# Kernel optimization log

Hardware: AMD Instinct MI355X
Metric: run time of the kernel (lower is better)

## Reference

```python
import jax, jax.numpy as jnp
import numpy as np

BAND_WIDTH = 0.5
EPS = 1e-5
NORM_EPS = 1e-12  # F.normalize eps


def setup_inputs() -> dict:
    key = jax.random.key(0)
    k1, k2 = jax.random.split(key)
    shape = (8, 512, 48, 48)  # N, C, H, W  (VGG conv4_4 features of a 384x384 image)
    return {
        "pred": jax.random.normal(k1, shape, dtype=jnp.float32),
        "target": jax.random.normal(k2, shape, dtype=jnp.float32),
    }


def reference(pred, target):
    N, C, H, W = pred.shape
    # center both by target channel-mean over (N, H, W)
    y_mu = jnp.mean(target, axis=(0, 2, 3), keepdims=True)
    x_c = pred - y_mu
    y_c = target - y_mu
    # L2-normalize along channel dim (F.normalize: divide by max(norm, eps))
    x_n = x_c / jnp.maximum(jnp.linalg.norm(x_c, axis=1, keepdims=True), NORM_EPS)
    y_n = y_c / jnp.maximum(jnp.linalg.norm(y_c, axis=1, keepdims=True), NORM_EPS)
    x_v = x_n.reshape(N, C, H * W)
    y_v = y_n.reshape(N, C, H * W)
    # pairwise cosine distance: [N, HW, HW]
    cosine_sim = jnp.einsum('ncp,ncq->npq', x_v, y_v)
    dist_raw = 1.0 - cosine_sim
    # relative distance: divide each row by its min over keys (dim=2)
    dist_min = jnp.min(dist_raw, axis=2, keepdims=True)
    dist_tilde = dist_raw / (dist_min + EPS)
    # similarity + row-normalize (softmax-like over dim=2)
    w = jnp.exp((1.0 - dist_tilde) / BAND_WIDTH)
    cx = w / jnp.sum(w, axis=2, keepdims=True)
    # max over query dim (dim=1), mean over key dim -> [N]
    cx = jnp.mean(jnp.max(cx, axis=1), axis=1)
    cx_loss = -jnp.log(cx + EPS)
    # reduction='mean', loss_weight=1.0
    return jnp.mean(cx_loss)
```

## Files before the change

### kernel.cpp

```cpp
#include <hip/hip_runtime.h>
#include <stdint.h>

#define NB 8
#define CC 512
#define PP 2304
#define EPSF 1e-5f

typedef short bf16x8 __attribute__((ext_vector_type(8)));
typedef float f32x4 __attribute__((ext_vector_type(4)));

__device__ __forceinline__ float bf2f(uint32_t b16) {
  return __uint_as_float(b16 << 16);
}
__device__ __forceinline__ uint32_t f2bf(float f) {
  uint32_t u = __float_as_uint(f);
  return (u + 0x7fffu + ((u >> 16) & 1u)) >> 16;
}

__global__ __launch_bounds__(256) void k_chan_mean(const float* __restrict__ tgt,
                                                   float* __restrict__ mu) {
  const int c = blockIdx.x, t = threadIdx.x;
  float s = 0.f;
  for (int n = 0; n < NB; ++n) {
    const float* b = tgt + ((size_t)n * CC + c) * PP;
    for (int p = t; p < PP; p += 256) s += b[p];
  }
  for (int off = 32; off; off >>= 1) s += __shfl_down(s, off);
  __shared__ float red[4];
  if ((t & 63) == 0) red[t >> 6] = s;
  __syncthreads();
  if (t == 0) mu[c] = (red[0] + red[1] + red[2] + red[3]) * (1.0f / (NB * PP));
}

__global__ __launch_bounds__(256) void k_center_cast(
    const float* __restrict__ pred, const float* __restrict__ tgt,
    const float* __restrict__ mu,
    uint16_t* __restrict__ xt, uint16_t* __restrict__ yt,
    float* __restrict__ ssx, float* __restrict__ ssy) {
  __shared__ uint32_t lt[64][33];
  __shared__ float red[4][64];
  const int p0 = blockIdx.x * 64, c0 = blockIdx.y * 64, n = blockIdx.z;
  const int t = threadIdx.x, lp = t & 63, cb = t >> 6;
  for (int which = 0; which < 2; ++which) {
    const float* in = which ? tgt : pred;
    uint16_t* out = which ? yt : xt;
    float* ss = which ? ssy : ssx;
    float sq = 0.f;
    uint32_t packs[8];
#pragma unroll
    for (int i = 0; i < 16; ++i) {
      const int c = c0 + cb * 16 + i;
      float v = in[((size_t)n * CC + c) * PP + p0 + lp] - mu[c];
      sq += v * v;
      uint32_t b = f2bf(v);
      if (i & 1) packs[i >> 1] |= b << 16; else packs[i >> 1] = b;
    }
#pragma unroll
    for (int j = 0; j < 8; ++j) lt[lp][cb * 8 + j] = packs[j];
    red[cb][lp] = sq;
    __syncthreads();
    if (t < 64)
      atomicAdd(&ss[(size_t)n * PP + p0 + t],
                red[0][t] + red[1][t] + red[2][t] + red[3][t]);
    const int p = t >> 2, ch = t & 3;
    uint4 v0, v1;
    v0.x = lt[p][ch * 8 + 0]; v0.y = lt[p][ch * 8 + 1];
    v0.z = lt[p][ch * 8 + 2]; v0.w = lt[p][ch * 8 + 3];
    v1.x = lt[p][ch * 8 + 4]; v1.y = lt[p][ch * 8 + 5];
    v1.z = lt[p][ch * 8 + 6]; v1.w = lt[p][ch * 8 + 7];
    uint4* ob = (uint4*)(out + (((size_t)n * PP + p0 + p) * CC + c0 + ch * 16));
    ob[0] = v0; ob[1] = v1;
    __syncthreads();
  }
}

__global__ __launch_bounds__(256) void k_invnorm(const float* __restrict__ ss,
                                                 float* __restrict__ inv) {
  int i = blockIdx.x * 256 + threadIdx.x;
  if (i < 2 * NB * PP) inv[i] = 1.0f / fmaxf(sqrtf(ss[i]), 1e-12f);
}

__global__ __launch_bounds__(256) void k_gemm(
    const uint16_t* __restrict__ xt, const uint16_t* __restrict__ yt,
    const float* __restrict__ invx, const float* __restrict__ invy,
    uint16_t* __restrict__ S) {
  __shared__ uint16_t As[128 * 64];
  __shared__ uint16_t Bs[128 * 64];
  const int nb = blockIdx.z;
  const int m0 = blockIdx.x * 128, n0 = blockIdx.y * 128;
  const int t = threadIdx.x, lane = t & 63, wid = t >> 6;
  const int wr = wid >> 1, wc = wid & 1;
  const uint16_t* Ax = xt + (size_t)nb * PP * CC;
  const uint16_t* By = yt + (size_t)nb * PP * CC;
  const int ric = lane >> 3;
  const int slot = lane & 7;
  f32x4 acc[4][4];
#pragma unroll
  for (int i = 0; i < 4; ++i)
#pragma unroll
    for (int j = 0; j < 4; ++j) acc[i][j] = (f32x4){0.f, 0.f, 0.f, 0.f};

  for (int k0 = 0; k0 < CC; k0 += 64) {
    __syncthreads();
#pragma unroll
    for (int j = 0; j < 4; ++j) {
      const int row = (wid * 4 + j) * 8 + ric;
      const int ssw = (slot ^ (row & 7)) << 4;
      uint4 va = *(const uint4*)(Ax + (size_t)(m0 + row) * CC + k0 + slot * 8);
      uint4 vb = *(const uint4*)(By + (size_t)(n0 + row) * CC + k0 + slot * 8);
      *(uint4*)((char*)As + row * 128 + ssw) = va;
      *(uint4*)((char*)Bs + row * 128 + ssw) = vb;
    }
    __syncthreads();
#pragma unroll
    for (int kk = 0; kk < 2; ++kk) {
      const int kb = kk * 64 + (lane >> 4) * 16;
      bf16x8 af[4], bfr[4];
#pragma unroll
      for (int mi = 0; mi < 4; ++mi) {
        const int row = wr * 64 + mi * 16 + (lane & 15);
        af[mi] = *(const bf16x8*)((const char*)As + row * 128 + (kb ^ ((row & 7) << 4)));
      }
#pragma unroll
      for (int ni = 0; ni < 4; ++ni) {
        const int row = wc * 64 + ni * 16 + (lane & 15);
        bfr[ni] = *(const bf16x8*)((const char*)Bs + row * 128 + (kb ^ ((row & 7) << 4)));
      }
#pragma unroll
      for (int mi = 0; mi < 4; ++mi)
#pragma unroll
        for (int ni = 0; ni < 4; ++ni)
          acc[mi][ni] = __builtin_amdgcn_mfma_f32_16x16x32_bf16(
              af[mi], bfr[ni], acc[mi][ni], 0, 0, 0);
    }
  }
  const float* rip = invx + (size_t)nb * PP;
  const float* cip = invy + (size_t)nb * PP;
  float rinv[4][4], cinv[4];
#pragma unroll
  for (int mi = 0; mi < 4; ++mi)
#pragma unroll
    for (int r = 0; r < 4; ++r)
      rinv[mi][r] = rip[m0 + wr * 64 + mi * 16 + (lane >> 4) * 4 + r];
#pragma unroll
  for (int ni = 0; ni < 4; ++ni)
    cinv[ni] = cip[n0 + wc * 64 + ni * 16 + (lane & 15)];
  uint16_t* Sp = S + (size_t)nb * PP * PP;
#pragma unroll
  for (int mi = 0; mi < 4; ++mi) {
#pragma unroll
    for (int r = 0; r < 4; ++r) {
      const int grow = m0 + wr * 64 + mi * 16 + (lane >> 4) * 4 + r;
      uint16_t* rowp = Sp + (size_t)grow * PP + n0 + wc * 64 + (lane & 15);
#pragma unroll
      for (int ni = 0; ni < 4; ++ni) {
        float v = acc[mi][ni][r] * rinv[mi][r] * cinv[ni];
        rowp[ni * 16] = (uint16_t)f2bf(v);
      }
    }
  }
}

__global__ __launch_bounds__(256) void k_rowstats(const uint16_t* __restrict__ S,
                                                  float* __restrict__ dmin,
                                                  float* __restrict__ rsum) {
  const int row = blockIdx.x;
  const uint32_t* Sp = (const uint32_t*)(S + (size_t)row * PP);
  __shared__ float cosr[PP];
  __shared__ float reda[4], redb[4];
  const int t = threadIdx.x;
  float mx = -2.f;
  for (int i = t; i < PP / 2; i += 256) {
    uint32_t u = Sp[i];
    float a = bf2f(u & 0xffffu), b = bf2f(u >> 16);
    *(float2*)&cosr[2 * i] = make_float2(a, b);
    mx = fmaxf(mx, fmaxf(a, b));
  }
  for (int off = 32; off; off >>= 1) mx = fmaxf(mx, __shfl_down(mx, off));
  if ((t & 63) == 0) reda[t >> 6] = mx;
  __syncthreads();
  mx = fmaxf(fmaxf(reda[0], reda[1]), fmaxf(reda[2], reda[3]));
  const float dm = 1.0f - mx;
  const float sc = 2.0f / (dm + EPSF);
  float s = 0.f;
  for (int i = t; i < PP; i += 256) s += __expf((cosr[i] - mx + EPSF) * sc);
  for (int off = 32; off; off >>= 1) s += __shfl_down(s, off);
  if ((t & 63) == 0) redb[t >> 6] = s;
  __syncthreads();
  if (t == 0) { dmin[row] = dm; rsum[row] = redb[0] + redb[1] + redb[2] + redb[3]; }
}

__global__ __launch_bounds__(256) void k_colmax_part(const uint16_t* __restrict__ S,
                                                     const float* __restrict__ dmin,
                                                     const float* __restrict__ rsum,
                                                     float* __restrict__ pcm) {
  const int n = blockIdx.y, pc = blockIdx.z, t = threadIdx.x;
  const int q = blockIdx.x * 256 + t;
  __shared__ float lmx[384], lsc[384], lri[384];
  const float* dmn = dmin + (size_t)n * PP;
  const float* rsn = rsum + (size_t)n * PP;
  for (int i = t; i < 384; i += 256) {
    float dm = dmn[pc * 384 + i];
    lmx[i] = 1.0f - dm - EPSF;
    lsc[i] = 2.0f / (dm + EPSF);
    lri[i] = 1.0f / rsn[pc * 384 + i];
  }
  __syncthreads();
  const uint16_t* Sn = S + (size_t)n * PP * PP + (size_t)pc * 384 * PP + q;
  float best = 0.f;
  for (int p = 0; p < 384; ++p) {
    float c = bf2f((uint32_t)Sn[(size_t)p * PP]);
    best = fmaxf(best, __expf((c - lmx[p]) * lsc[p]) * lri[p]);
  }
  pcm[((size_t)n * 6 + pc) * PP + q] = best;
}

__global__ __launch_bounds__(256) void k_colmax_fin(const float* __restrict__ pcm,
                                                    float* __restrict__ cxacc) {
  const int n = blockIdx.y, t = threadIdx.x;
  const int q = blockIdx.x * 256 + t;
  float best = 0.f;
  for (int c = 0; c < 6; ++c) best = fmaxf(best, pcm[((size_t)n * 6 + c) * PP + q]);
  float s = best;
  for (int off = 32; off; off >>= 1) s += __shfl_down(s, off);
  __shared__ float red[4];
  if ((t & 63) == 0) red[t >> 6] = s;
  __syncthreads();
  if (t == 0) atomicAdd(&cxacc[n], red[0] + red[1] + red[2] + red[3]);
}

__global__ void k_final(const float* __restrict__ cxacc, float* __restrict__ out) {
  if (threadIdx.x == 0 && blockIdx.x == 0) {
    float s = 0.f;
    for (int n = 0; n < NB; ++n) {
      float cx = cxacc[n] * (1.0f / PP);
      s += -logf(cx + EPSF);
    }
    out[0] = s * (1.0f / NB);
  }
}

extern "C" void kernel_launch(void* const* d_in, const int* in_sizes, int n_in,
                              void* d_out, int out_size, void* d_ws, size_t ws_size,
                              hipStream_t stream) {
  const float* pred = (const float*)d_in[0];
  const float* tgt  = (const float*)d_in[1];
  float* W = (float*)d_ws;
  float* mu   = W + 0;
  float* ssx  = W + 1024;
  float* ssy  = W + 19456;
  float* cx   = W + 37888;
  float* invx = W + 38400;
  float* invy = W + 56832;
  float* dmin = W + 75264;
  float* rsum = W + 93696;
  float* pcm  = W + 112640;
  uint16_t* xt = (uint16_t*)(W + 223744);
  uint16_t* yt = xt + (size_t)NB * PP * CC;
  uint16_t* S  = yt + (size_t)NB * PP * CC;

  hipMemsetAsync(W + 1024, 0, (36872) * sizeof(float), stream);

  k_chan_mean<<<dim3(CC), dim3(256), 0, stream>>>(tgt, mu);
  k_center_cast<<<dim3(PP / 64, CC / 64, NB), dim3(256), 0, stream>>>(
      pred, tgt, mu, xt, yt, ssx, ssy);
  k_invnorm<<<dim3((2 * NB * PP) / 256), dim3(256), 0, stream>>>(ssx, invx);
  k_gemm<<<dim3(PP / 128, PP / 128, NB), dim3(256), 0, stream>>>(xt, yt, invx, invy, S);
  k_rowstats<<<dim3(NB * PP), dim3(256), 0, stream>>>(S, dmin, rsum);
  k_colmax_part<<<dim3(PP / 256, NB, 6), dim3(256), 0, stream>>>(S, dmin, rsum, pcm);
  k_colmax_fin<<<dim3(PP / 256, NB), dim3(256), 0, stream>>>(pcm, cx);
  k_final<<<1, 64, 0, stream>>>(cx, (float*)d_out);
}
```

Baseline: 191.5 us.

## Use async global-to-LDS loads in GEMM, fold invnorm, widen row/column kernels

The GEMM now stages tiles with global_load_lds async copies using a pre-swizzled source address instead of register round-trips. It also remaps block IDs so each XCD handles one batch, and computes the inverse norms inline, which removes the k_invnorm launch. The rowstats kernel reads 4 bf16 values per load. The column-max partial kernel processes two columns per thread with 32-bit loads across 12 row chunks, and its partial buffer is reused from the xt region. These changes target launch overhead, load width, and L2 locality, at the cost of more partial results to reduce and a dependence on xt being dead after the GEMM.

Result: faster. 170.7 us (-10.9%).

```diff
diff --git a/kernel.cpp b/kernel.cpp
--- a/kernel.cpp
+++ b/kernel.cpp
@@ -5,9 +5,18 @@
 #define CC 512
 #define PP 2304
 #define EPSF 1e-5f
+#define NPC 12
+#define PCH 192
 
 typedef short bf16x8 __attribute__((ext_vector_type(8)));
 typedef float f32x4 __attribute__((ext_vector_type(4)));
+
+typedef __attribute__((address_space(3))) uint8_t lds8_t;
+typedef __attribute__((address_space(1))) const uint8_t g8_t;
+
+__device__ __forceinline__ void async16(void* lds, const void* g) {
+  __builtin_amdgcn_global_load_lds((g8_t*)g, (lds8_t*)lds, 16, 0, 0);
+}
 
 __device__ __forceinline__ float bf2f(uint32_t b16) {
   return __uint_as_float(b16 << 16);
@@ -74,26 +83,33 @@
   }
 }
 
-__global__ __launch_bounds__(256) void k_invnorm(const float* __restrict__ ss,
-                                                 float* __restrict__ inv) {
-  int i = blockIdx.x * 256 + threadIdx.x;
-  if (i < 2 * NB * PP) inv[i] = 1.0f / fmaxf(sqrtf(ss[i]), 1e-12f);
-}
-
 __global__ __launch_bounds__(256) void k_gemm(
     const uint16_t* __restrict__ xt, const uint16_t* __restrict__ yt,
-    const float* __restrict__ invx, const float* __restrict__ invy,
+    const float* __restrict__ ssx, const float* __restrict__ ssy,
     uint16_t* __restrict__ S) {
   __shared__ uint16_t As[128 * 64];
   __shared__ uint16_t Bs[128 * 64];
-  const int nb = blockIdx.z;
-  const int m0 = blockIdx.x * 128, n0 = blockIdx.y * 128;
+  int flat = blockIdx.x + 18 * blockIdx.y + 324 * blockIdx.z;
+  flat = (flat & 7) * 324 + (flat >> 3);
+  const int nb = flat / 324;
+  const int rem = flat - nb * 324;
+  const int byn = rem / 18;
+  const int bxm = rem - byn * 18;
+  const int m0 = bxm * 128, n0 = byn * 128;
   const int t = threadIdx.x, lane = t & 63, wid = t >> 6;
   const int wr = wid >> 1, wc = wid & 1;
   const uint16_t* Ax = xt + (size_t)nb * PP * CC;
   const uint16_t* By = yt + (size_t)nb * PP * CC;
-  const int ric = lane >> 3;
-  const int slot = lane & 7;
+  const int lrow = lane >> 3;
+  const int lswz = (lane & 7) ^ lrow;
+  const uint16_t* gA[4];
+  const uint16_t* gB[4];
+#pragma unroll
+  for (int j = 0; j < 4; ++j) {
+    const int row = (wid * 4 + j) * 8 + lrow;
+    gA[j] = Ax + (size_t)(m0 + row) * CC + lswz * 8;
+    gB[j] = By + (size_t)(n0 + row) * CC + lswz * 8;
+  }
   f32x4 acc[4][4];
 #pragma unroll
   for (int i = 0; i < 4; ++i)
@@ -104,12 +120,8 @@
     __syncthreads();
 #pragma unroll
     for (int j = 0; j < 4; ++j) {
-      const int row = (wid * 4 + j) * 8 + ric;
-      const int ssw = (slot ^ (row & 7)) << 4;
-      uint4 va = *(const uint4*)(Ax + (size_t)(m0 + row) * CC + k0 + slot * 8);
-      uint4 vb = *(const uint4*)(By + (size_t)(n0 + row) * CC + k0 + slot * 8);
-      *(uint4*)((char*)As + row * 128 + ssw) = va;
-      *(uint4*)((char*)Bs + row * 128 + ssw) = vb;
+      async16(As + (wid * 4 + j) * 512, gA[j] + k0);
+      async16(Bs + (wid * 4 + j) * 512, gB[j] + k0);
     }
     __syncthreads();
 #pragma unroll
@@ -134,17 +146,17 @@
               af[mi], bfr[ni], acc[mi][ni], 0, 0, 0);
     }
   }
-  const float* rip = invx + (size_t)nb * PP;
-  const float* cip = invy + (size_t)nb * PP;
+  const float* rsp = ssx + (size_t)nb * PP;
+  const float* csp = ssy + (size_t)nb * PP;
   float rinv[4][4], cinv[4];
 #pragma unroll
   for (int mi = 0; mi < 4; ++mi)
 #pragma unroll
     for (int r = 0; r < 4; ++r)
-      rinv[mi][r] = rip[m0 + wr * 64 + mi * 16 + (lane >> 4) * 4 + r];
+      rinv[mi][r] = 1.0f / fmaxf(sqrtf(rsp[m0 + wr * 64 + mi * 16 + (lane >> 4) * 4 + r]), 1e-12f);
 #pragma unroll
   for (int ni = 0; ni < 4; ++ni)
-    cinv[ni] = cip[n0 + wc * 64 + ni * 16 + (lane & 15)];
+    cinv[ni] = 1.0f / fmaxf(sqrtf(csp[n0 + wc * 64 + ni * 16 + (lane & 15)]), 1e-12f);
   uint16_t* Sp = S + (size_t)nb * PP * PP;
 #pragma unroll
   for (int mi = 0; mi < 4; ++mi) {
@@ -165,16 +177,17 @@
                                                   float* __restrict__ dmin,
                                                   float* __restrict__ rsum) {
   const int row = blockIdx.x;
-  const uint32_t* Sp = (const uint32_t*)(S + (size_t)row * PP);
-  __shared__ float cosr[PP];
+  const uint2* Sp = (const uint2*)(S + (size_t)row * PP);
+  __shared__ __align__(16) float cosr[PP];
   __shared__ float reda[4], redb[4];
   const int t = threadIdx.x;
   float mx = -2.f;
-  for (int i = t; i < PP / 2; i += 256) {
-    uint32_t u = Sp[i];
-    float a = bf2f(u & 0xffffu), b = bf2f(u >> 16);
-    *(float2*)&cosr[2 * i] = make_float2(a, b);
-    mx = fmaxf(mx, fmaxf(a, b));
+  for (int i = t; i < PP / 4; i += 256) {
+    uint2 u = Sp[i];
+    float a = bf2f(u.x & 0xffffu), b = bf2f(u.x >> 16);
+    float c = bf2f(u.y & 0xffffu), d = bf2f(u.y >> 16);
+    *(float4*)&cosr[4 * i] = make_float4(a, b, c, d);
+    mx = fmaxf(fmaxf(mx, fmaxf(a, b)), fmaxf(c, d));
   }
   for (int off = 32; off; off >>= 1) mx = fmaxf(mx, __shfl_down(mx, off));
   if ((t & 63) == 0) reda[t >> 6] = mx;
@@ -195,24 +208,30 @@
                                                      const float* __restrict__ rsum,
                                                      float* __restrict__ pcm) {
   const int n = blockIdx.y, pc = blockIdx.z, t = threadIdx.x;
-  const int q = blockIdx.x * 256 + t;
-  __shared__ float lmx[384], lsc[384], lri[384];
-  const float* dmn = dmin + (size_t)n * PP;
-  const float* rsn = rsum + (size_t)n * PP;
-  for (int i = t; i < 384; i += 256) {
-    float dm = dmn[pc * 384 + i];
+  const int q2 = blockIdx.x * 512 + 2 * t;
+  __shared__ float lmx[PCH], lsc[PCH], lri[PCH];
+  const float* dmn = dmin + (size_t)n * PP + pc * PCH;
+  const float* rsn = rsum + (size_t)n * PP + pc * PCH;
+  for (int i = t; i < PCH; i += 256) {
+    float dm = dmn[i];
     lmx[i] = 1.0f - dm - EPSF;
     lsc[i] = 2.0f / (dm + EPSF);
-    lri[i] = 1.0f / rsn[pc * 384 + i];
-  }
-  __syncthreads();
-  const uint16_t* Sn = S + (size_t)n * PP * PP + (size_t)pc * 384 * PP + q;
-  float best = 0.f;
-  for (int p = 0; p < 384; ++p) {
-    float c = bf2f((uint32_t)Sn[(size_t)p * PP]);
-    best = fmaxf(best, __expf((c - lmx[p]) * lsc[p]) * lri[p]);
-  }
-  pcm[((size_t)n * 6 + pc) * PP + q] = best;
+    lri[i] = 1.0f / rsn[i];
+  }
+  __syncthreads();
+  if (q2 >= PP) return;
+  const uint32_t* Sn =
+      (const uint32_t*)(S + (size_t)n * PP * PP + (size_t)pc * PCH * PP + q2);
+  float b0 = 0.f, b1 = 0.f;
+#pragma unroll 8
+  for (int p = 0; p < PCH; ++p) {
+    uint32_t u = Sn[(size_t)p * (PP / 2)];
+    float mxv = lmx[p], scv = lsc[p], riv = lri[p];
+    b0 = fmaxf(b0, __expf((bf2f(u & 0xffffu) - mxv) * scv) * riv);
+    b1 = fmaxf(b1, __expf((bf2f(u >> 16) - mxv) * scv) * riv);
+  }
+  float* o = pcm + ((size_t)n * NPC + pc) * PP + q2;
+  o[0] = b0; o[1] = b1;
 }
 
 __global__ __launch_bounds__(256) void k_colmax_fin(const float* __restrict__ pcm,
@@ -220,7 +239,8 @@
   const int n = blockIdx.y, t = threadIdx.x;
   const int q = blockIdx.x * 256 + t;
   float best = 0.f;
-  for (int c = 0; c < 6; ++c) best = fmaxf(best, pcm[((size_t)n * 6 + c) * PP + q]);
+#pragma unroll
+  for (int c = 0; c < NPC; ++c) best = fmaxf(best, pcm[((size_t)n * NPC + c) * PP + q]);
   float s = best;
   for (int off = 32; off; off >>= 1) s += __shfl_down(s, off);
   __shared__ float red[4];
@@ -250,24 +270,22 @@
   float* ssx  = W + 1024;
   float* ssy  = W + 19456;
   float* cx   = W + 37888;
-  float* invx = W + 38400;
-  float* invy = W + 56832;
   float* dmin = W + 75264;
   float* rsum = W + 93696;
-  float* pcm  = W + 112640;
   uint16_t* xt = (uint16_t*)(W + 223744);
   uint16_t* yt = xt + (size_t)NB * PP * CC;
   uint16_t* S  = yt + (size_t)NB * PP * CC;
+  float* pcm = (float*)xt;
 
   hipMemsetAsync(W + 1024, 0, (36872) * sizeof(float), stream);
 
   k_chan_mean<<<dim3(CC), dim3(256), 0, stream>>>(tgt, mu);
   k_center_cast<<<dim3(PP / 64, CC / 64, NB), dim3(256), 0, stream>>>(
       pred, tgt, mu, xt, yt, ssx, ssy);
-  k_invnorm<<<dim3((2 * NB * PP) / 256), dim3(256), 0, stream>>>(ssx, invx);
-  k_gemm<<<dim3(PP / 128, PP / 128, NB), dim3(256), 0, stream>>>(xt, yt, invx, invy, S);
+  k_gemm<<<dim3(PP / 128, PP / 128, NB), dim3(256), 0, stream>>>(xt, yt, ssx, ssy, S);
   k_rowstats<<<dim3(NB * PP), dim3(256), 0, stream>>>(S, dmin, rsum);
-  k_colmax_part<<<dim3(PP / 256, NB, 6), dim3(256), 0, stream>>>(S, dmin, rsum, pcm);
+  k_colmax_part<<<dim3((PP + 511) / 512, NB, NPC), dim3(256), 0, stream>>>(
+      S, dmin, rsum, pcm);
   k_colmax_fin<<<dim3(PP / 256, NB), dim3(256), 0, stream>>>(pcm, cx);
   k_final<<<1, 64, 0, stream>>>(cx, (float*)d_out);
 }
```
